# Performance work log

Hardware: AMD Instinct MI355X
Metric: run time of the kernel (lower is better)

The kernel has to match this reference:

```python
import jax, jax.numpy as jnp
import numpy as np

N_NODES = 50000
N_EDGES = 800000
IN_F = 256
OUT_F = 64


def setup_inputs() -> dict:
    key = jax.random.key(0)
    k1, k2, k3, k4, k5 = jax.random.split(key, 5)
    x = jax.random.normal(k1, (N_NODES, IN_F), dtype=jnp.float32)
    # xavier-uniform-like init for weight
    limit = float(np.sqrt(6.0 / (IN_F + OUT_F)))
    weight = jax.random.uniform(k2, (IN_F, OUT_F), dtype=jnp.float32, minval=-limit, maxval=limit)
    bias = jnp.zeros((1, OUT_F), dtype=jnp.float32)
    edge_weight = jax.random.uniform(k3, (N_EDGES,), dtype=jnp.float32)
    edge_src = jax.random.randint(k4, (N_EDGES,), 0, N_NODES, dtype=jnp.int32)
    edge_dst = jax.random.randint(k5, (N_EDGES,), 0, N_NODES, dtype=jnp.int32)
    return {"x": x, "weight": weight, "bias": bias,
            "edge_weight": edge_weight, "edge_src": edge_src, "edge_dst": edge_dst}


def reference(x, weight, bias, edge_weight, edge_src, edge_dst):
    # in_features (256) > out_features (64): transform first, then propagate.
    h = x @ weight                                  # [N, out]
    # spmm with COO adjacency: out[dst] += w_e * h[src]
    msgs = h[edge_src] * edge_weight[:, None]       # [E, out]
    out = jax.ops.segment_sum(msgs, edge_dst, num_segments=x.shape[0])  # [N, out]
    return out + bias
```

## Files before the change

kernel.cpp:

```cpp
#include <hip/hip_runtime.h>
#include <hip/hip_bf16.h>

#define N_NODES 50000
#define N_EDGES 800000
#define IN_F 256
#define OUT_F 64

#define CAP 64
#define NBKT 256
#define DST_PER_BKT 196
#define NPERM 50176
#define BKT_CAP 3584

typedef __attribute__((ext_vector_type(8))) short short8;
typedef __attribute__((ext_vector_type(4))) float f32x4;

static __device__ __forceinline__ ushort f2bf(float v) {
    __hip_bfloat16 b = __float2bfloat16(v);
    return *(ushort*)&b;
}

__global__ __launch_bounds__(256) void gc_prep(const float* __restrict__ W,
                                               ushort* __restrict__ Wb,
                                               int* __restrict__ cursor) {
    const int g = blockIdx.x * 256 + threadIdx.x;
    if (g < NBKT) cursor[g] = 0;
    {
        const int s = g >> 9;
        const int kk = (g >> 6) & 7;
        const int lane = g & 63;
        const int n = s * 16 + (lane & 15);
        const int kb = kk * 32 + (lane >> 4) * 8;
#pragma unroll
        for (int j = 0; j < 8; ++j)
            Wb[(size_t)g * 8 + j] = f2bf(W[(kb + j) * OUT_F + n]);
    }
}

__global__ __launch_bounds__(256) void gc_bucket(const int* __restrict__ esrc,
                                                 const int* __restrict__ edst,
                                                 const float* __restrict__ ew,
                                                 int* __restrict__ cursor,
                                                 uint2* __restrict__ arena) {
    __shared__ int hist[NBKT];
    __shared__ int base[NBKT];
    const int t = threadIdx.x;
    hist[t] = 0;
    __syncthreads();

    const int e0 = blockIdx.x * 2048 + t * 8;
    const bool valid = e0 < N_EDGES;
    int b[8], loff[8];
    uint2 ent[8];
    if (valid) {
        const int4 sa = *(const int4*)(esrc + e0);
        const int4 sb = *(const int4*)(esrc + e0 + 4);
        const int4 da = *(const int4*)(edst + e0);
        const int4 db = *(const int4*)(edst + e0 + 4);
        const float4 wa = *(const float4*)(ew + e0);
        const float4 wb = *(const float4*)(ew + e0 + 4);
        const int ds[8] = {da.x, da.y, da.z, da.w, db.x, db.y, db.z, db.w};
        const int ss[8] = {sa.x, sa.y, sa.z, sa.w, sb.x, sb.y, sb.z, sb.w};
        const float wf[8] = {wa.x, wa.y, wa.z, wa.w, wb.x, wb.y, wb.z, wb.w};
#pragma unroll
        for (int j = 0; j < 8; ++j) {
            b[j] = ds[j] / DST_PER_BKT;
            ent[j].x = (unsigned)ds[j];
            ent[j].y = ((unsigned)f2bf(wf[j]) << 16) | (unsigned)(ss[j] & 0xFFFF);
            loff[j] = atomicAdd(&hist[b[j]], 1);
        }
    }
    __syncthreads();
    {
        const int hc = hist[t];
        base[t] = hc ? atomicAdd(&cursor[t], hc) : 0;
    }
    __syncthreads();
    if (valid) {
#pragma unroll
        for (int j = 0; j < 8; ++j) {
            const int pos = base[b[j]] + loff[j];
            if (pos < BKT_CAP)
                arena[(size_t)b[j] * BKT_CAP + pos] = ent[j];
        }
    }
}

__global__ __launch_bounds__(512) void gc_place2(const uint2* __restrict__ arena,
                                                 const int* __restrict__ cursor,
                                                 int* __restrict__ cnt,
                                                 unsigned int* __restrict__ slots,
                                                 int* __restrict__ perm) {
    __shared__ int lcnt[DST_PER_BKT];
    __shared__ int dhist[CAP + 1];
    const int b = blockIdx.x;
    const int t = threadIdx.x;
    const int dbase = b * DST_PER_BKT;

    if (t < DST_PER_BKT) lcnt[t] = 0;
    if (t >= 512 - (CAP + 1)) dhist[t - (512 - (CAP + 1))] = 0;
    __syncthreads();

    const int n = min(cursor[b], BKT_CAP);
    const uint2* __restrict__ p = arena + (size_t)b * BKT_CAP;
    for (int i = t; i < n; i += 1024) {
        const uint2 e0 = p[i];
        const bool has1 = (i + 512) < n;
        uint2 e1 = {0u, 0u};
        if (has1) e1 = p[i + 512];
        const int pos0 = atomicAdd(&lcnt[e0.x - dbase], 1);
        if (pos0 < CAP) slots[(size_t)e0.x * CAP + pos0] = e0.y;
        if (has1) {
            const int pos1 = atomicAdd(&lcnt[e1.x - dbase], 1);
            if (pos1 < CAP) slots[(size_t)e1.x * CAP + pos1] = e1.y;
        }
    }
    __syncthreads();

    if (t < DST_PER_BKT) {
        const int d = dbase + t;
        if (d < N_NODES) cnt[d] = lcnt[t];
        atomicAdd(&dhist[min(lcnt[t], CAP)], 1);
    }
    __syncthreads();
    if (t == 0) {
        int run = 0;
#pragma unroll
        for (int k = 0; k <= CAP; ++k) { const int c = dhist[k]; dhist[k] = run; run += c; }
    }
    __syncthreads();
    if (t < DST_PER_BKT) {
        const int rank = atomicAdd(&dhist[min(lcnt[t], CAP)], 1);
        perm[dbase + rank] = dbase + t;
    }
}

__global__ __launch_bounds__(256) void gc_gemm(const float* __restrict__ x,
                                               const ushort* __restrict__ Wb,
                                               ushort* __restrict__ h) {
    __shared__ ushort xs[32 * 264];
    const int t = threadIdx.x;
    const int nbase = blockIdx.x * 32;

    {
#pragma unroll
        for (int i = 0; i < 8; ++i) {
            const int idx = t + i * 256;
            const int node = idx >> 6;
            const int c4 = idx & 63;
            int gnode = nbase + node;
            if (gnode >= N_NODES) gnode = N_NODES - 1;
            const float4 v = ((const float4*)x)[(size_t)gnode * 64 + c4];
            ushort4 bv;
            bv.x = f2bf(v.x); bv.y = f2bf(v.y); bv.z = f2bf(v.z); bv.w = f2bf(v.w);
            *(ushort4*)&xs[node * 264 + c4 * 4] = bv;
        }
    }

    const int s = t >> 6;
    const int lane = t & 63;
    const int m = lane & 15;
    const int quad = lane >> 4;

    short8 bfrag[8];
#pragma unroll
    for (int kk = 0; kk < 8; ++kk)
        bfrag[kk] = *(const short8*)(Wb + ((size_t)(s * 8 + kk) * 64 + lane) * 8);

    __syncthreads();

    f32x4 acc0 = {0.f, 0.f, 0.f, 0.f};
    f32x4 acc1 = {0.f, 0.f, 0.f, 0.f};
#pragma unroll
    for (int kk = 0; kk < 8; ++kk) {
        const short8 a0 = *(const short8*)&xs[m * 264 + kk * 32 + quad * 8];
        const short8 a1 = *(const short8*)&xs[(16 + m) * 264 + kk * 32 + quad * 8];
        acc0 = __builtin_amdgcn_mfma_f32_16x16x32_bf16(a0, bfrag[kk], acc0, 0, 0, 0);
        acc1 = __builtin_amdgcn_mfma_f32_16x16x32_bf16(a1, bfrag[kk], acc1, 0, 0, 0);
    }

#pragma unroll
    for (int r = 0; r < 4; ++r) {
        const int row0 = nbase + quad * 4 + r;
        const int row1 = row0 + 16;
        if (row0 < N_NODES) h[(size_t)row0 * OUT_F + s * 16 + m] = f2bf(acc0[r]);
        if (row1 < N_NODES) h[(size_t)row1 * OUT_F + s * 16 + m] = f2bf(acc1[r]);
    }
}

__global__ __launch_bounds__(256) void gc_gather(const ushort* __restrict__ h,
                                                 const unsigned int* __restrict__ slots,
                                                 const int* __restrict__ cnt,
                                                 const int* __restrict__ perm,
                                                 const float* __restrict__ bias,
                                                 float* __restrict__ out) {
    const int wid = (blockIdx.x * 256 + threadIdx.x) >> 6;
    const int l = threadIdx.x & 63;
    const int base = wid * 8;

    int pdv = 0, dgv = 0;
    if (l < 8) {
        pdv = perm[base + l];
        dgv = (pdv < N_NODES) ? min(cnt[pdv], CAP) : 0;
    }
    const int pd0 = __builtin_amdgcn_readlane(pdv, 0);
    const int pd1 = __builtin_amdgcn_readlane(pdv, 1);
    const int pd2 = __builtin_amdgcn_readlane(pdv, 2);
    const int pd3 = __builtin_amdgcn_readlane(pdv, 3);
    const int pd4 = __builtin_amdgcn_readlane(pdv, 4);
    const int pd5 = __builtin_amdgcn_readlane(pdv, 5);
    const int pd6 = __builtin_amdgcn_readlane(pdv, 6);
    const int pd7 = __builtin_amdgcn_readlane(pdv, 7);
    const int dg0 = __builtin_amdgcn_readlane(dgv, 0);
    const int dg1 = __builtin_amdgcn_readlane(dgv, 1);
    const int dg2 = __builtin_amdgcn_readlane(dgv, 2);
    const int dg3 = __builtin_amdgcn_readlane(dgv, 3);
    const int dg4 = __builtin_amdgcn_readlane(dgv, 4);
    const int dg5 = __builtin_amdgcn_readlane(dgv, 5);
    const int dg6 = __builtin_amdgcn_readlane(dgv, 6);
    const int dg7 = __builtin_amdgcn_readlane(dgv, 7);
    const int mdeg = max(max(max(dg0, dg1), max(dg2, dg3)),
                         max(max(dg4, dg5), max(dg6, dg7)));

    const unsigned sw0 = (l < dg0) ? slots[(size_t)pd0 * CAP + l] : 0u;
    const unsigned sw1 = (l < dg1) ? slots[(size_t)pd1 * CAP + l] : 0u;
    const unsigned sw2 = (l < dg2) ? slots[(size_t)pd2 * CAP + l] : 0u;
    const unsigned sw3 = (l < dg3) ? slots[(size_t)pd3 * CAP + l] : 0u;
    const unsigned sw4 = (l < dg4) ? slots[(size_t)pd4 * CAP + l] : 0u;
    const unsigned sw5 = (l < dg5) ? slots[(size_t)pd5 * CAP + l] : 0u;
    const unsigned sw6 = (l < dg6) ? slots[(size_t)pd6 * CAP + l] : 0u;
    const unsigned sw7 = (l < dg7) ? slots[(size_t)pd7 * CAP + l] : 0u;

    const float bf = bias[l];
    float a0 = bf, a1 = bf, a2 = bf, a3 = bf, a4 = bf, a5 = bf, a6 = bf, a7 = bf;

    const ushort* __restrict__ hf = h + l;

#define ROWLD(sw, ll) \
    hf[(size_t)((unsigned)__builtin_amdgcn_readlane((int)(sw), (ll)) & 0xFFFFu) * OUT_F]
#define WBITS(sw, ll) \
    __uint_as_float((unsigned)__builtin_amdgcn_readlane((int)(sw), (ll)) & 0xFFFF0000u)

    for (int i0 = 0; i0 < mdeg; i0 += 8) {
        unsigned hv0[8], hv1[8], hv2[8], hv3[8], hv4[8], hv5[8], hv6[8], hv7[8];
#pragma unroll
        for (int j = 0; j < 8; ++j) {
            const int ll = i0 + j;
            hv0[j] = ROWLD(sw0, ll);
            hv1[j] = ROWLD(sw1, ll);
            hv2[j] = ROWLD(sw2, ll);
            hv3[j] = ROWLD(sw3, ll);
            hv4[j] = ROWLD(sw4, ll);
            hv5[j] = ROWLD(sw5, ll);
            hv6[j] = ROWLD(sw6, ll);
            hv7[j] = ROWLD(sw7, ll);
        }
#pragma unroll
        for (int j = 0; j < 8; ++j) {
            const int ll = i0 + j;
            a0 += WBITS(sw0, ll) * __uint_as_float(hv0[j] << 16);
            a1 += WBITS(sw1, ll) * __uint_as_float(hv1[j] << 16);
            a2 += WBITS(sw2, ll) * __uint_as_float(hv2[j] << 16);
            a3 += WBITS(sw3, ll) * __uint_as_float(hv3[j] << 16);
            a4 += WBITS(sw4, ll) * __uint_as_float(hv4[j] << 16);
            a5 += WBITS(sw5, ll) * __uint_as_float(hv5[j] << 16);
            a6 += WBITS(sw6, ll) * __uint_as_float(hv6[j] << 16);
            a7 += WBITS(sw7, ll) * __uint_as_float(hv7[j] << 16);
        }
    }
#undef ROWLD
#undef WBITS

    if (pd0 < N_NODES) out[(size_t)pd0 * OUT_F + l] = a0;
    if (pd1 < N_NODES) out[(size_t)pd1 * OUT_F + l] = a1;
    if (pd2 < N_NODES) out[(size_t)pd2 * OUT_F + l] = a2;
    if (pd3 < N_NODES) out[(size_t)pd3 * OUT_F + l] = a3;
    if (pd4 < N_NODES) out[(size_t)pd4 * OUT_F + l] = a4;
    if (pd5 < N_NODES) out[(size_t)pd5 * OUT_F + l] = a5;
    if (pd6 < N_NODES) out[(size_t)pd6 * OUT_F + l] = a6;
    if (pd7 < N_NODES) out[(size_t)pd7 * OUT_F + l] = a7;
}

extern "C" void kernel_launch(void* const* d_in, const int* in_sizes, int n_in,
                              void* d_out, int out_size, void* d_ws, size_t ws_size,
                              hipStream_t stream) {
    const float* x    = (const float*)d_in[0];
    const float* W    = (const float*)d_in[1];
    const float* bias = (const float*)d_in[2];
    const float* ew   = (const float*)d_in[3];
    const int* src    = (const int*)d_in[4];
    const int* dst    = (const int*)d_in[5];
    float* out = (float*)d_out;

    char* ws = (char*)d_ws;
    ushort* h           = (ushort*)ws;
    int* cnt            = (int*)(ws + 6400000);
    unsigned int* slots = (unsigned int*)(ws + 6600000);
    ushort* Wb          = (ushort*)(ws + 19400000);
    int* cursor         = (int*)(ws + 19432768);
    int* perm           = (int*)(ws + 19433792);
    uint2* arena        = (uint2*)(ws + 19634496);

    gc_prep<<<8, 256, 0, stream>>>(W, Wb, cursor);
    gc_bucket<<<391, 256, 0, stream>>>(src, dst, ew, cursor, arena);
    gc_place2<<<NBKT, 512, 0, stream>>>(arena, cursor, cnt, slots, perm);
    gc_gemm<<<1563, 256, 0, stream>>>(x, Wb, h);
    gc_gather<<<1568, 256, 0, stream>>>(h, slots, cnt, perm, bias, out);
}
```

Baseline: 141.4 us.

## Co-schedule GEMM tiles with bucketing and placement kernels via block-range dispatch

Splits the dense x@W GEMM into two halves and merges each half into the bucket and place kernels as extra blocks. Each fused launch branches on block index, so the edge-sorting work and the GEMM run concurrently instead of serially. This removes one launch and lets memory-bound sorting overlap with GEMM work. The cost is that the place stage now uses 256 threads per block instead of 512, and every block reserves the union of the shared memory of both roles, which may lower occupancy.

Result: no change. 143.7 us (+1.6%).

```diff
diff --git a/kernel.cpp b/kernel.cpp
--- a/kernel.cpp
+++ b/kernel.cpp
@@ -9,7 +9,6 @@
 #define CAP 64
 #define NBKT 256
 #define DST_PER_BKT 196
-#define NPERM 50176
 #define BKT_CAP 3584
 
 typedef __attribute__((ext_vector_type(8))) short short8;
@@ -18,6 +17,57 @@
 static __device__ __forceinline__ ushort f2bf(float v) {
     __hip_bfloat16 b = __float2bfloat16(v);
     return *(ushort*)&b;
+}
+
+static __device__ __forceinline__ void gemm_tile(const float* __restrict__ x,
+                                                 const ushort* __restrict__ Wb,
+                                                 ushort* __restrict__ h,
+                                                 const int nbase, const int t,
+                                                 ushort* __restrict__ xs) {
+    {
+#pragma unroll
+        for (int i = 0; i < 8; ++i) {
+            const int idx = t + i * 256;
+            const int node = idx >> 6;
+            const int c4 = idx & 63;
+            int gnode = nbase + node;
+            if (gnode >= N_NODES) gnode = N_NODES - 1;
+            const float4 v = ((const float4*)x)[(size_t)gnode * 64 + c4];
+            ushort4 bv;
+            bv.x = f2bf(v.x); bv.y = f2bf(v.y); bv.z = f2bf(v.z); bv.w = f2bf(v.w);
+            *(ushort4*)&xs[node * 264 + c4 * 4] = bv;
+        }
+    }
+
+    const int s = t >> 6;
+    const int lane = t & 63;
+    const int m = lane & 15;
+    const int quad = lane >> 4;
+
+    short8 bfrag[8];
+#pragma unroll
+    for (int kk = 0; kk < 8; ++kk)
+        bfrag[kk] = *(const short8*)(Wb + ((size_t)(s * 8 + kk) * 64 + lane) * 8);
+
+    __syncthreads();
+
+    f32x4 acc0 = {0.f, 0.f, 0.f, 0.f};
+    f32x4 acc1 = {0.f, 0.f, 0.f, 0.f};
+#pragma unroll
+    for (int kk = 0; kk < 8; ++kk) {
+        const short8 a0 = *(const short8*)&xs[m * 264 + kk * 32 + quad * 8];
+        const short8 a1 = *(const short8*)&xs[(16 + m) * 264 + kk * 32 + quad * 8];
+        acc0 = __builtin_amdgcn_mfma_f32_16x16x32_bf16(a0, bfrag[kk], acc0, 0, 0, 0);
+        acc1 = __builtin_amdgcn_mfma_f32_16x16x32_bf16(a1, bfrag[kk], acc1, 0, 0, 0);
+    }
+
+#pragma unroll
+    for (int r = 0; r < 4; ++r) {
+        const int row0 = nbase + quad * 4 + r;
+        const int row1 = row0 + 16;
+        if (row0 < N_NODES) h[(size_t)row0 * OUT_F + s * 16 + m] = f2bf(acc0[r]);
+        if (row1 < N_NODES) h[(size_t)row1 * OUT_F + s * 16 + m] = f2bf(acc1[r]);
+    }
 }
 
 __global__ __launch_bounds__(256) void gc_prep(const float* __restrict__ W,
@@ -37,155 +87,122 @@
     }
 }
 
-__global__ __launch_bounds__(256) void gc_bucket(const int* __restrict__ esrc,
-                                                 const int* __restrict__ edst,
-                                                 const float* __restrict__ ew,
-                                                 int* __restrict__ cursor,
-                                                 uint2* __restrict__ arena) {
+__global__ __launch_bounds__(256) void gc_mid1(const float* __restrict__ x,
+                                               const ushort* __restrict__ Wb,
+                                               ushort* __restrict__ h,
+                                               const int* __restrict__ esrc,
+                                               const int* __restrict__ edst,
+                                               const float* __restrict__ ew,
+                                               int* __restrict__ cursor,
+                                               uint2* __restrict__ arena) {
+    __shared__ ushort xs[32 * 264];
     __shared__ int hist[NBKT];
     __shared__ int base[NBKT];
     const int t = threadIdx.x;
-    hist[t] = 0;
-    __syncthreads();
-
-    const int e0 = blockIdx.x * 2048 + t * 8;
-    const bool valid = e0 < N_EDGES;
-    int b[8], loff[8];
-    uint2 ent[8];
-    if (valid) {
-        const int4 sa = *(const int4*)(esrc + e0);
-        const int4 sb = *(const int4*)(esrc + e0 + 4);
-        const int4 da = *(const int4*)(edst + e0);
-        const int4 db = *(const int4*)(edst + e0 + 4);
-        const float4 wa = *(const float4*)(ew + e0);
-        const float4 wb = *(const float4*)(ew + e0 + 4);
-        const int ds[8] = {da.x, da.y, da.z, da.w, db.x, db.y, db.z, db.w};
-        const int ss[8] = {sa.x, sa.y, sa.z, sa.w, sb.x, sb.y, sb.z, sb.w};
-        const float wf[8] = {wa.x, wa.y, wa.z, wa.w, wb.x, wb.y, wb.z, wb.w};
-#pragma unroll
-        for (int j = 0; j < 8; ++j) {
-            b[j] = ds[j] / DST_PER_BKT;
-            ent[j].x = (unsigned)ds[j];
-            ent[j].y = ((unsigned)f2bf(wf[j]) << 16) | (unsigned)(ss[j] & 0xFFFF);
-            loff[j] = atomicAdd(&hist[b[j]], 1);
-        }
-    }
-    __syncthreads();
-    {
-        const int hc = hist[t];
-        base[t] = hc ? atomicAdd(&cursor[t], hc) : 0;
-    }
-    __syncthreads();
-    if (valid) {
-#pragma unroll
-        for (int j = 0; j < 8; ++j) {
-            const int pos = base[b[j]] + loff[j];
-            if (pos < BKT_CAP)
-                arena[(size_t)b[j] * BKT_CAP + pos] = ent[j];
-        }
-    }
-}
-
-__global__ __launch_bounds__(512) void gc_place2(const uint2* __restrict__ arena,
-                                                 const int* __restrict__ cursor,
-                                                 int* __restrict__ cnt,
-                                                 unsigned int* __restrict__ slots,
-                                                 int* __restrict__ perm) {
+
+    if (blockIdx.x < 391) {
+        hist[t] = 0;
+        __syncthreads();
+
+        const int e0 = blockIdx.x * 2048 + t * 8;
+        const bool valid = e0 < N_EDGES;
+        int b[8], loff[8];
+        uint2 ent[8];
+        if (valid) {
+            const int4 sa = *(const int4*)(esrc + e0);
+            const int4 sb = *(const int4*)(esrc + e0 + 4);
+            const int4 da = *(const int4*)(edst + e0);
+            const int4 db = *(const int4*)(edst + e0 + 4);
+            const float4 wa = *(const float4*)(ew + e0);
+            const float4 wb = *(const float4*)(ew + e0 + 4);
+            const int ds[8] = {da.x, da.y, da.z, da.w, db.x, db.y, db.z, db.w};
+            const int ss[8] = {sa.x, sa.y, sa.z, sa.w, sb.x, sb.y, sb.z, sb.w};
+            const float wf[8] = {wa.x, wa.y, wa.z, wa.w, wb.x, wb.y, wb.z, wb.w};
+#pragma unroll
+            for (int j = 0; j < 8; ++j) {
+                b[j] = ds[j] / DST_PER_BKT;
+                ent[j].x = (unsigned)ds[j];
+                ent[j].y = ((unsigned)f2bf(wf[j]) << 16) | (unsigned)(ss[j] & 0xFFFF);
+                loff[j] = atomicAdd(&hist[b[j]], 1);
+            }
+        }
+        __syncthreads();
+        {
+            const int hc = hist[t];
+            base[t] = hc ? atomicAdd(&cursor[t], hc) : 0;
+        }
+        __syncthreads();
+        if (valid) {
+#pragma unroll
+            for (int j = 0; j < 8; ++j) {
+                const int pos = base[b[j]] + loff[j];
+                if (pos < BKT_CAP)
+                    arena[(size_t)b[j] * BKT_CAP + pos] = ent[j];
+            }
+        }
+        return;
+    }
+
+    gemm_tile(x, Wb, h, (blockIdx.x - 391) * 32, t, xs);
+}
+
+__global__ __launch_bounds__(256) void gc_mid2(const float* __restrict__ x,
+                                               const ushort* __restrict__ Wb,
+                                               ushort* __restrict__ h,
+                                               const uint2* __restrict__ arena,
+                                               const int* __restrict__ cursor,
+                                               int* __restrict__ cnt,
+                                               unsigned int* __restrict__ slots,
+                                               int* __restrict__ perm) {
+    __shared__ ushort xs[32 * 264];
     __shared__ int lcnt[DST_PER_BKT];
     __shared__ int dhist[CAP + 1];
-    const int b = blockIdx.x;
     const int t = threadIdx.x;
-    const int dbase = b * DST_PER_BKT;
-
-    if (t < DST_PER_BKT) lcnt[t] = 0;
-    if (t >= 512 - (CAP + 1)) dhist[t - (512 - (CAP + 1))] = 0;
-    __syncthreads();
-
-    const int n = min(cursor[b], BKT_CAP);
-    const uint2* __restrict__ p = arena + (size_t)b * BKT_CAP;
-    for (int i = t; i < n; i += 1024) {
-        const uint2 e0 = p[i];
-        const bool has1 = (i + 512) < n;
-        uint2 e1 = {0u, 0u};
-        if (has1) e1 = p[i + 512];
-        const int pos0 = atomicAdd(&lcnt[e0.x - dbase], 1);
-        if (pos0 < CAP) slots[(size_t)e0.x * CAP + pos0] = e0.y;
-        if (has1) {
-            const int pos1 = atomicAdd(&lcnt[e1.x - dbase], 1);
-            if (pos1 < CAP) slots[(size_t)e1.x * CAP + pos1] = e1.y;
-        }
-    }
-    __syncthreads();
-
-    if (t < DST_PER_BKT) {
-        const int d = dbase + t;
-        if (d < N_NODES) cnt[d] = lcnt[t];
-        atomicAdd(&dhist[min(lcnt[t], CAP)], 1);
-    }
-    __syncthreads();
-    if (t == 0) {
-        int run = 0;
-#pragma unroll
-        for (int k = 0; k <= CAP; ++k) { const int c = dhist[k]; dhist[k] = run; run += c; }
-    }
-    __syncthreads();
-    if (t < DST_PER_BKT) {
-        const int rank = atomicAdd(&dhist[min(lcnt[t], CAP)], 1);
-        perm[dbase + rank] = dbase + t;
-    }
-}
-
-__global__ __launch_bounds__(256) void gc_gemm(const float* __restrict__ x,
-                                               const ushort* __restrict__ Wb,
-                                               ushort* __restrict__ h) {
-    __shared__ ushort xs[32 * 264];
-    const int t = threadIdx.x;
-    const int nbase = blockIdx.x * 32;
-
-    {
-#pragma unroll
-        for (int i = 0; i < 8; ++i) {
-            const int idx = t + i * 256;
-            const int node = idx >> 6;
-            const int c4 = idx & 63;
-            int gnode = nbase + node;
-            if (gnode >= N_NODES) gnode = N_NODES - 1;
-            const float4 v = ((const float4*)x)[(size_t)gnode * 64 + c4];
-            ushort4 bv;
-            bv.x = f2bf(v.x); bv.y = f2bf(v.y); bv.z = f2bf(v.z); bv.w = f2bf(v.w);
-            *(ushort4*)&xs[node * 264 + c4 * 4] = bv;
-        }
-    }
-
-    const int s = t >> 6;
-    const int lane = t & 63;
-    const int m = lane & 15;
-    const int quad = lane >> 4;
-
-    short8 bfrag[8];
-#pragma unroll
-    for (int kk = 0; kk < 8; ++kk)
-        bfrag[kk] = *(const short8*)(Wb + ((size_t)(s * 8 + kk) * 64 + lane) * 8);
-
-    __syncthreads();
-
-    f32x4 acc0 = {0.f, 0.f, 0.f, 0.f};
-    f32x4 acc1 = {0.f, 0.f, 0.f, 0.f};
-#pragma unroll
-    for (int kk = 0; kk < 8; ++kk) {
-        const short8 a0 = *(const short8*)&xs[m * 264 + kk * 32 + quad * 8];
-        const short8 a1 = *(const short8*)&xs[(16 + m) * 264 + kk * 32 + quad * 8];
-        acc0 = __builtin_amdgcn_mfma_f32_16x16x32_bf16(a0, bfrag[kk], acc0, 0, 0, 0);
-        acc1 = __builtin_amdgcn_mfma_f32_16x16x32_bf16(a1, bfrag[kk], acc1, 0, 0, 0);
-    }
-
-#pragma unroll
-    for (int r = 0; r < 4; ++r) {
-        const int row0 = nbase + quad * 4 + r;
-        const int row1 = row0 + 16;
-        if (row0 < N_NODES) h[(size_t)row0 * OUT_F + s * 16 + m] = f2bf(acc0[r]);
-        if (row1 < N_NODES) h[(size_t)row1 * OUT_F + s * 16 + m] = f2bf(acc1[r]);
-    }
+
+    if (blockIdx.x < NBKT) {
+        const int b = blockIdx.x;
+        const int dbase = b * DST_PER_BKT;
+
+        if (t < DST_PER_BKT) lcnt[t] = 0;
+        if (t >= 256 - (CAP + 1)) dhist[t - (256 - (CAP + 1))] = 0;
+        __syncthreads();
+
+        const int n = min(cursor[b], BKT_CAP);
+        const uint2* __restrict__ p = arena + (size_t)b * BKT_CAP;
+        for (int i = t; i < n; i += 512) {
+            const uint2 e0 = p[i];
+            const bool has1 = (i + 256) < n;
+            uint2 e1 = {0u, 0u};
+            if (has1) e1 = p[i + 256];
+            const int pos0 = atomicAdd(&lcnt[e0.x - dbase], 1);
+            if (pos0 < CAP) slots[(size_t)e0.x * CAP + pos0] = e0.y;
+            if (has1) {
+                const int pos1 = atomicAdd(&lcnt[e1.x - dbase], 1);
+                if (pos1 < CAP) slots[(size_t)e1.x * CAP + pos1] = e1.y;
+            }
+        }
+        __syncthreads();
+
+        if (t < DST_PER_BKT) {
+            const int d = dbase + t;
+            if (d < N_NODES) cnt[d] = lcnt[t];
+            atomicAdd(&dhist[min(lcnt[t], CAP)], 1);
+        }
+        __syncthreads();
+        if (t == 0) {
+            int run = 0;
+#pragma unroll
+            for (int k = 0; k <= CAP; ++k) { const int c = dhist[k]; dhist[k] = run; run += c; }
+        }
+        __syncthreads();
+        if (t < DST_PER_BKT) {
+            const int rank = atomicAdd(&dhist[min(lcnt[t], CAP)], 1);
+            perm[dbase + rank] = dbase + t;
+        }
+        return;
+    }
+
+    gemm_tile(x, Wb, h, (blockIdx.x - NBKT + 782) * 32, t, xs);
 }
 
 __global__ __launch_bounds__(256) void gc_gather(const ushort* __restrict__ h,
@@ -302,8 +319,7 @@
     uint2* arena        = (uint2*)(ws + 19634496);
 
     gc_prep<<<8, 256, 0, stream>>>(W, Wb, cursor);
-    gc_bucket<<<391, 256, 0, stream>>>(src, dst, ew, cursor, arena);
-    gc_place2<<<NBKT, 512, 0, stream>>>(arena, cursor, cnt, slots, perm);
-    gc_gemm<<<1563, 256, 0, stream>>>(x, Wb, h);
+    gc_mid1<<<1173, 256, 0, stream>>>(x, Wb, h, src, dst, ew, cursor, arena);
+    gc_mid2<<<1037, 256, 0, stream>>>(x, Wb, h, arena, cursor, cnt, slots, perm);
     gc_gather<<<1568, 256, 0, stream>>>(h, slots, cnt, perm, bias, out);
 }
```
